# Performance work log

Measured on AMD Instinct MI355X. Metric: run time of the kernel, lower is better.

## Reference

```python
import jax, jax.numpy as jnp
import numpy as np

B, L, HID, NH, HD = 1, 2304, 3072, 24, 128
IMG = 2048
MLP = 4 * HID  # 12288
EPS = 1e-6


def _layernorm(x):
    mu = jnp.mean(x, axis=-1, keepdims=True)
    var = jnp.mean(jnp.square(x - mu), axis=-1, keepdims=True)
    return (x - mu) * jax.lax.rsqrt(var + EPS)


def _rmsnorm(x, w):
    ms = jnp.mean(jnp.square(x), axis=-1, keepdims=True)
    return x * jax.lax.rsqrt(ms + EPS) * w


def _rope_interleaved(x, cos, sin):
    # x: [B, S, H, D]; cos/sin: [1, S, 1, D] with pairwise-equal values (mode=1, GPT-J)
    x1 = x[..., 0::2]
    x2 = x[..., 1::2]
    c = cos[..., 0::2]
    s = sin[..., 0::2]
    even = x1 * c - x2 * s
    odd = x1 * s + x2 * c
    return jnp.stack([even, odd], axis=-1).reshape(x.shape)


def setup_inputs() -> dict:
    key = jax.random.key(0)
    ks = jax.random.split(key, 10)
    scale_in = 1.0 / np.sqrt(HID)
    x = jax.random.normal(ks[0], (B, L, HID), jnp.float32)
    vec = jax.random.normal(ks[1], (B, HID), jnp.float32)
    # RoPE tables (interleaved layout: value repeated per pair)
    pos = jnp.arange(IMG, dtype=jnp.float32)
    inv_freq = 1.0 / (10000.0 ** (jnp.arange(HD // 2, dtype=jnp.float32) / (HD // 2)))
    ang = pos[:, None] * inv_freq[None, :]               # [IMG, HD/2]
    freqs_cos = jnp.repeat(jnp.cos(ang), 2, axis=-1).reshape(1, IMG, 1, HD)
    freqs_sin = jnp.repeat(jnp.sin(ang), 2, axis=-1).reshape(1, IMG, 1, HD)
    mod_w = jax.random.normal(ks[2], (HID, 3 * HID), jnp.float32) * scale_in
    mod_b = jnp.zeros((3 * HID,), jnp.float32)
    w1 = jax.random.normal(ks[3], (HID, 3 * HID + MLP), jnp.float32) * scale_in
    b1 = jnp.zeros((3 * HID + MLP,), jnp.float32)
    q_norm_w = jnp.ones((HD,), jnp.float32)
    k_norm_w = jnp.ones((HD,), jnp.float32)
    w2 = jax.random.normal(ks[4], (HID + MLP, HID), jnp.float32) * (1.0 / np.sqrt(HID + MLP))
    b2 = jnp.zeros((HID,), jnp.float32)
    return {
        'x': x, 'vec': vec, 'img_len': IMG,
        'freqs_cos': freqs_cos, 'freqs_sin': freqs_sin,
        'mod_w': mod_w, 'mod_b': mod_b, 'w1': w1, 'b1': b1,
        'q_norm_w': q_norm_w, 'k_norm_w': k_norm_w, 'w2': w2, 'b2': b2,
    }


def reference(x, vec, img_len, freqs_cos, freqs_sin, mod_w, mod_b, w1, b1,
              q_norm_w, k_norm_w, w2, b2):
    # modulation: SiLU(vec) -> Linear -> shift/scale/gate  [B, HID] each
    mod = jax.nn.silu(vec) @ mod_w + mod_b
    shift, scale, gate = jnp.split(mod, 3, axis=-1)
    x_mod = _layernorm(x) * (1.0 + scale[:, None, :]) + shift[:, None, :]

    # fused QKV + MLP projection
    proj = x_mod @ w1 + b1                                  # [B, L, 3*HID + MLP]
    qkv, mlp = proj[..., :3 * HID], proj[..., 3 * HID:]
    q, k, v = [t[:, :, 0] for t in [None]] if False else None, None, None
    qkv = qkv.reshape(B, L, 3, NH, HD)
    q, k, v = qkv[:, :, 0], qkv[:, :, 1], qkv[:, :, 2]      # [B, L, NH, HD]

    q = _rmsnorm(q, q_norm_w)
    k = _rmsnorm(k, k_norm_w)

    # RoPE only on image tokens
    q = jnp.concatenate([_rope_interleaved(q[:, :img_len], freqs_cos, freqs_sin), q[:, img_len:]], axis=1)
    k = jnp.concatenate([_rope_interleaved(k[:, :img_len], freqs_cos, freqs_sin), k[:, img_len:]], axis=1)

    # full (img+txt) bidirectional attention
    attn_scale = 1.0 / np.sqrt(HD)
    scores = jnp.einsum('blhd,bmhd->bhlm', q, k) * attn_scale
    probs = jax.nn.softmax(scores, axis=-1)
    attn = jnp.einsum('bhlm,bmhd->blhd', probs, v).reshape(B, L, NH * HD)

    # output fusion: [attn | gelu_tanh(mlp)] @ w2
    out = jnp.concatenate([attn, jax.nn.gelu(mlp, approximate=True)], axis=-1) @ w2 + b2
    return x + out * gate[:, None, :]
```

## Files before the change

kernel.cpp:

```cpp
#include <hip/hip_runtime.h>

#define L_SEQ 2304
#define HID_D 3072
#define NH_D 24
#define HD_D 128
#define N1_D 21504
#define QKVN 9216
#define K2_D 15360
#define EPS_V 1e-6f
#define ATTN_SC 0.08838834764831843f

typedef __bf16 bf16x8 __attribute__((ext_vector_type(8)));
typedef float f32x4 __attribute__((ext_vector_type(4)));
typedef unsigned int u32x4 __attribute__((ext_vector_type(4)));
typedef unsigned short u16x8 __attribute__((ext_vector_type(8)));
typedef unsigned short u16x4 __attribute__((ext_vector_type(4)));

#define WAITVM(N) asm volatile("s_waitcnt vmcnt(" #N ")" ::: "memory")
#define LGKM0 asm volatile("s_waitcnt lgkmcnt(0)" ::: "memory")
#define SB0 __builtin_amdgcn_sched_barrier(0)

__device__ __forceinline__ unsigned short f2bf(float f) {
  unsigned int u = __builtin_bit_cast(unsigned int, f);
  u += 0x7fffu + ((u >> 16) & 1u);
  return (unsigned short)(u >> 16);
}

__device__ __forceinline__ float gelu_f(float x) {
  float u = 0.7978845608028654f * (x + 0.044715f * x * x * x);
  float e = __expf(2.f * u);
  float th = 1.f - 2.f / (e + 1.f);
  return 0.5f * x * (1.f + th);
}

__device__ __forceinline__ void gload16(const void* g, void* l) {
  __builtin_amdgcn_global_load_lds(
      (const __attribute__((address_space(1))) unsigned int*)g,
      (__attribute__((address_space(3))) unsigned int*)l, 16, 0, 0);
}

__global__ __launch_bounds__(256) void mod_partial_kernel(
    const float* __restrict__ vec, const float* __restrict__ mod_w,
    float* __restrict__ partial) {
  __shared__ float s[384];
  const int t = threadIdx.x;
  const int kb = blockIdx.y;
  const int k0 = kb * 384;
  for (int p = t; p < 384; p += 256) {
    float v = vec[k0 + p];
    s[p] = v / (1.f + __expf(-v));
  }
  __syncthreads();
  const int n = blockIdx.x * 256 + t;
  float acc = 0.f;
  const float* wp = mod_w + (size_t)k0 * QKVN + n;
#pragma unroll 4
  for (int j = 0; j < 384; ++j) acc += s[j] * wp[(size_t)j * QKVN];
  partial[kb * QKVN + n] = acc;
}

__global__ __launch_bounds__(256) void mod_reduce_kernel(
    const float* __restrict__ partial, const float* __restrict__ mod_b,
    float* __restrict__ mod) {
  const int n = blockIdx.x * 256 + threadIdx.x;
  float acc = mod_b[n];
#pragma unroll
  for (int i = 0; i < 8; ++i) acc += partial[i * QKVN + n];
  mod[n] = acc;
}

__global__ __launch_bounds__(256) void ln_mod_kernel(
    const float* __restrict__ x, const float* __restrict__ mod,
    unsigned short* __restrict__ xmod) {
  const int row = blockIdx.x;
  const int t = threadIdx.x;
  const float* xr = x + (size_t)row * HID_D;
  float4 v[3];
  float sum = 0.f, sq = 0.f;
#pragma unroll
  for (int p = 0; p < 3; ++p) {
    v[p] = *(const float4*)&xr[p * 1024 + t * 4];
    sum += v[p].x + v[p].y + v[p].z + v[p].w;
    sq += v[p].x * v[p].x + v[p].y * v[p].y + v[p].z * v[p].z + v[p].w * v[p].w;
  }
#pragma unroll
  for (int o = 1; o < 64; o <<= 1) {
    sum += __shfl_xor(sum, o);
    sq += __shfl_xor(sq, o);
  }
  __shared__ float rs[8];
  const int w = t >> 6;
  if ((t & 63) == 0) { rs[w] = sum; rs[4 + w] = sq; }
  __syncthreads();
  sum = rs[0] + rs[1] + rs[2] + rs[3];
  sq = rs[4] + rs[5] + rs[6] + rs[7];
  const float mu = sum * (1.f / HID_D);
  const float var = sq * (1.f / HID_D) - mu * mu;
  const float rstd = rsqrtf(var + EPS_V);
#pragma unroll
  for (int p = 0; p < 3; ++p) {
    const int c = p * 1024 + t * 4;
    float4 sc = *(const float4*)&mod[3072 + c];
    float4 sh = *(const float4*)&mod[c];
    u16x4 o4;
    o4[0] = f2bf((v[p].x - mu) * rstd * (1.f + sc.x) + sh.x);
    o4[1] = f2bf((v[p].y - mu) * rstd * (1.f + sc.y) + sh.y);
    o4[2] = f2bf((v[p].z - mu) * rstd * (1.f + sc.z) + sh.z);
    o4[3] = f2bf((v[p].w - mu) * rstd * (1.f + sc.w) + sh.w);
    *(u16x4*)&xmod[(size_t)row * HID_D + c] = o4;
  }
}

__global__ __launch_bounds__(256) void convert_transpose_kernel(
    const float* __restrict__ src, unsigned short* __restrict__ dst,
    const int K, const int N) {
  __shared__ unsigned short lt[64][72];
  const int t = threadIdx.x;
  const int n0 = blockIdx.x * 64;
  const int k0 = blockIdx.y * 64;
  const int kr = t >> 4;
  const int n4 = (t & 15) * 4;
#pragma unroll
  for (int p = 0; p < 4; ++p) {
    const int k = kr + p * 16;
    float4 v = *(const float4*)&src[(size_t)(k0 + k) * N + n0 + n4];
    lt[n4 + 0][k] = f2bf(v.x);
    lt[n4 + 1][k] = f2bf(v.y);
    lt[n4 + 2][k] = f2bf(v.z);
    lt[n4 + 3][k] = f2bf(v.w);
  }
  __syncthreads();
  const int nr = t >> 2;
  const int kc = (t & 3) * 16;
  u16x8 a = *(const u16x8*)&lt[nr][kc];
  u16x8 b = *(const u16x8*)&lt[nr][kc + 8];
  unsigned short* dp = &dst[(size_t)(n0 + nr) * K + k0 + kc];
  *(u16x8*)dp = a;
  *(u16x8*)(dp + 8) = b;
}

template <int BM>
__device__ __forceinline__ void gemm8_core(
    const unsigned short* __restrict__ A, const int lda,
    const unsigned short* __restrict__ B, const int ldb,
    const int m0, const int n0, const int nit, char* lds,
    f32x4 (*acc)[4]) {
  constexpr int AB = BM * 128;
  constexpr int AH = AB / 2;
  constexpr int BO = 2 * AB;
  constexpr int ALOADS = BM / 128;

  const int t = threadIdx.x;
  const int lane = t & 63;
  const int w = t >> 6;
  const int g = lane >> 4;
  const int c = lane & 15;
  const int wm = (w >> 2) * (BM / 2);
  const int wn = (w & 3) * 64;
  const int srow = w * 16 + (lane >> 2);
  const int scole = (lane & 3) * 8;

  auto stageA = [&](int buf, int kh, int kt) {
#pragma unroll
    for (int j = 0; j < ALOADS; ++j)
      gload16(A + (size_t)(m0 + j * 128 + srow) * lda + kt * 64 + kh * 32 + scole,
              lds + buf * AB + kh * AH + j * 8192 + w * 1024);
  };
  auto stageB = [&](int buf, int kh, int kt) {
#pragma unroll
    for (int j = 0; j < 2; ++j)
      gload16(B + (size_t)(n0 + j * 128 + srow) * ldb + kt * 64 + kh * 32 + scole,
              lds + BO + buf * 32768 + kh * 16384 + j * 8192 + w * 1024);
  };

  bf16x8 af[4], bf[4];
  auto loadA = [&](int buf, int mh, int kk) {
    const char* base = lds + buf * AB + kk * AH;
#pragma unroll
    for (int i = 0; i < 4; ++i)
      af[i] = *(const bf16x8*)(base + (wm + (mh * 4 + i) * 16 + c) * 64 + g * 16);
  };
  auto loadB4 = [&](int buf, int kk) {
    const char* base = lds + BO + buf * 32768 + kk * 16384;
#pragma unroll
    for (int i = 0; i < 4; ++i)
      bf[i] = *(const bf16x8*)(base + (wn + i * 16 + c) * 64 + g * 16);
  };
  auto loadB2 = [&](int buf, int hi, int kk) {
    const char* base = lds + BO + buf * 32768 + kk * 16384;
#pragma unroll
    for (int i = 0; i < 2; ++i)
      bf[hi * 2 + i] =
          *(const bf16x8*)(base + (wn + (hi * 2 + i) * 16 + c) * 64 + g * 16);
  };
  auto mfma16 = [&](int mb) {
#pragma unroll
    for (int i = 0; i < 4; ++i)
#pragma unroll
      for (int n = 0; n < 4; ++n)
        acc[mb + i][n] = __builtin_amdgcn_mfma_f32_16x16x32_bf16(
            af[i], bf[n], acc[mb + i][n], 0, 0, 0);
  };
  auto mfma8 = [&](int hi) {
#pragma unroll
    for (int i = 0; i < 4; ++i)
#pragma unroll
      for (int n = 0; n < 2; ++n)
        acc[i][hi * 2 + n] = __builtin_amdgcn_mfma_f32_16x16x32_bf16(
            af[i], bf[hi * 2 + n], acc[i][hi * 2 + n], 0, 0, 0);
  };
  auto mid = [&] {
    SB0;
    __builtin_amdgcn_s_barrier();
    LGKM0;
    SB0;
    __builtin_amdgcn_s_setprio(1);
  };
  auto end_nw = [&] {
    __builtin_amdgcn_s_setprio(0);
    SB0;
    __builtin_amdgcn_s_barrier();
  };

  stageA(0, 0, 0); stageB(0, 0, 0);
  stageA(0, 1, 0); stageB(0, 1, 0);
  stageA(1, 0, 1); stageB(1, 0, 1);
  if constexpr (BM == 256) WAITVM(8); else WAITVM(6);
  __builtin_amdgcn_s_barrier();

  for (int it = 0; it < nit; ++it) {
    const int t0 = 2 * it;
    const bool nl = (it + 1 < nit);
    if constexpr (BM == 256) { loadA(0, 0, 0); loadB4(0, 0); }
    else { loadA(0, 0, 0); loadB2(0, 0, 0); }
    stageA(1, 1, t0 + 1);
    mid();
    if constexpr (BM == 256) mfma16(0); else mfma8(0);
    end_nw();
    if constexpr (BM == 256) loadA(0, 1, 0); else loadB2(0, 1, 0);
    stageB(1, 1, t0 + 1);
    mid();
    if constexpr (BM == 256) mfma16(4); else mfma8(1);
    __builtin_amdgcn_s_setprio(0); SB0;
    if constexpr (BM == 256) WAITVM(8); else WAITVM(6);
    __builtin_amdgcn_s_barrier();
    if constexpr (BM == 256) { loadA(0, 0, 1); loadB4(0, 1); }
    else { loadA(0, 0, 1); loadB2(0, 0, 1); }
    if (nl) stageA(0, 0, t0 + 2);
    mid();
    if constexpr (BM == 256) mfma16(0); else mfma8(0);
    end_nw();
    if constexpr (BM == 256) loadA(0, 1, 1); else loadB2(0, 1, 1);
    if (nl) stageB(0, 0, t0 + 2);
    mid();
    if constexpr (BM == 256) mfma16(4); else mfma8(1);
    __builtin_amdgcn_s_setprio(0); SB0;
    if (nl) { if constexpr (BM == 256) WAITVM(8); else WAITVM(6); }
    else    { if constexpr (BM == 256) WAITVM(4); else WAITVM(3); }
    __builtin_amdgcn_s_barrier();
    if constexpr (BM == 256) { loadA(1, 0, 0); loadB4(1, 0); }
    else { loadA(1, 0, 0); loadB2(1, 0, 0); }
    if (nl) stageA(0, 1, t0 + 2);
    mid();
    if constexpr (BM == 256) mfma16(0); else mfma8(0);
    end_nw();
    if constexpr (BM == 256) loadA(1, 1, 0); else loadB2(1, 1, 0);
    if (nl) stageB(0, 1, t0 + 2);
    mid();
    if constexpr (BM == 256) mfma16(4); else mfma8(1);
    __builtin_amdgcn_s_setprio(0); SB0;
    if (nl) { if constexpr (BM == 256) WAITVM(8); else WAITVM(6); }
    else    { WAITVM(0); }
    __builtin_amdgcn_s_barrier();
    if constexpr (BM == 256) { loadA(1, 0, 1); loadB4(1, 1); }
    else { loadA(1, 0, 1); loadB2(1, 0, 1); }
    if (nl) stageA(1, 0, t0 + 3);
    mid();
    if constexpr (BM == 256) mfma16(0); else mfma8(0);
    end_nw();
    if constexpr (BM == 256) loadA(1, 1, 1); else loadB2(1, 1, 1);
    if (nl) stageB(1, 0, t0 + 3);
    mid();
    if constexpr (BM == 256) mfma16(4); else mfma8(1);
    __builtin_amdgcn_s_setprio(0); SB0;
    if (nl) { if constexpr (BM == 256) WAITVM(8); else WAITVM(6); }
    __builtin_amdgcn_s_barrier();
  }
}

__global__ __launch_bounds__(512, 2) void gemm1_kernel(
    const unsigned short* __restrict__ xmod, const unsigned short* __restrict__ w1t,
    const float* __restrict__ b1, float* __restrict__ qkv,
    unsigned short* __restrict__ hbuf) {
  __shared__ __align__(16) char smem[131072];
  f32x4 acc[8][4];
  const f32x4 zero = {0.f, 0.f, 0.f, 0.f};
#pragma unroll
  for (int i = 0; i < 8; ++i)
#pragma unroll
    for (int j = 0; j < 4; ++j) acc[i][j] = zero;
  const int orig = blockIdx.x;
  const int xcd = orig & 7;
  const int wgid = (xcd < 4 ? xcd * 95 : 380 + (xcd - 4) * 94) + (orig >> 3);
  const int m0 = (wgid % 9) * 256;
  const int n0 = (wgid / 9) * 256;
  gemm8_core<256>(xmod, HID_D, w1t, HID_D, m0, n0, 24, smem, acc);
  const int lane = threadIdx.x & 63;
  const int g = lane >> 4, c = lane & 15;
  const int w = threadIdx.x >> 6;
  const int wm = (w >> 2) * 128, wn = (w & 3) * 64;
  const bool is_mlp = (n0 >= QKVN);
#pragma unroll
  for (int mf = 0; mf < 8; ++mf)
#pragma unroll
    for (int nf = 0; nf < 4; ++nf)
#pragma unroll
      for (int j = 0; j < 4; ++j) {
        const int row = m0 + wm + mf * 16 + g * 4 + j;
        const int col = n0 + wn + nf * 16 + c;
        const float v = acc[mf][nf][j] + b1[col];
        if (!is_mlp) {
          qkv[(size_t)row * QKVN + col] = v;
        } else {
          hbuf[(size_t)row * K2_D + HID_D + (col - QKVN)] = f2bf(gelu_f(v));
        }
      }
}

__global__ __launch_bounds__(512, 2) void gemm2_kernel(
    const unsigned short* __restrict__ hbuf, const unsigned short* __restrict__ w2t,
    const float* __restrict__ b2, const float* __restrict__ x,
    const float* __restrict__ mod, float* __restrict__ out) {
  __shared__ __align__(16) char smem[98304];
  f32x4 acc[4][4];
  const f32x4 zero = {0.f, 0.f, 0.f, 0.f};
#pragma unroll
  for (int i = 0; i < 4; ++i)
#pragma unroll
    for (int j = 0; j < 4; ++j) acc[i][j] = zero;
  const int orig = blockIdx.x;
  const int wgid = (orig & 7) * 27 + (orig >> 3);
  const int m0 = (wgid % 18) * 128;
  const int n0 = (wgid / 18) * 256;
  gemm8_core<128>(hbuf, K2_D, w2t, K2_D, m0, n0, 120, smem, acc);
  const int lane = threadIdx.x & 63;
  const int g = lane >> 4, c = lane & 15;
  const int w = threadIdx.x >> 6;
  const int wm = (w >> 2) * 64, wn = (w & 3) * 64;
#pragma unroll
  for (int mf = 0; mf < 4; ++mf)
#pragma unroll
    for (int nf = 0; nf < 4; ++nf)
#pragma unroll
      for (int j = 0; j < 4; ++j) {
        const int row = m0 + wm + mf * 16 + g * 4 + j;
        const int col = n0 + wn + nf * 16 + c;
        const float v = acc[mf][nf][j] + b2[col];
        out[(size_t)row * HID_D + col] =
            x[(size_t)row * HID_D + col] + v * mod[6144 + col];
      }
}

__global__ __launch_bounds__(256) void qk_norm_rope_kernel(
    const float* __restrict__ qkv, const float* __restrict__ qw,
    const float* __restrict__ kw, const float* __restrict__ fc,
    const float* __restrict__ fs, const int* __restrict__ img_len_p,
    unsigned short* __restrict__ qr, unsigned short* __restrict__ kr) {
  const int l = blockIdx.x;
  const int t = threadIdx.x;
  const int wv = t >> 6;
  const int lane = t & 63;
  const int img = *img_len_p;
  const bool do_rope = (l < img);
  float cc = 1.f, ss = 0.f;
  if (do_rope) {
    cc = fc[l * HD_D + 2 * lane];
    ss = fs[l * HD_D + 2 * lane];
  }
  const float qw0 = qw[2 * lane], qw1 = qw[2 * lane + 1];
  const float kw0 = kw[2 * lane], kw1 = kw[2 * lane + 1];
#pragma unroll
  for (int hh = 0; hh < 6; ++hh) {
    const int h = hh * 4 + wv;
    {
      float2 q2 = *(const float2*)&qkv[(size_t)l * QKVN + h * HD_D + 2 * lane];
      float sq = q2.x * q2.x + q2.y * q2.y;
#pragma unroll
      for (int o = 1; o < 64; o <<= 1) sq += __shfl_xor(sq, o);
      const float r = rsqrtf(sq * (1.f / HD_D) + EPS_V);
      float a = q2.x * r * qw0, b = q2.y * r * qw1;
      float e = a, od = b;
      if (do_rope) { e = a * cc - b * ss; od = a * ss + b * cc; }
      e *= ATTN_SC; od *= ATTN_SC;
      unsigned int pk = (unsigned)f2bf(e) | ((unsigned)f2bf(od) << 16);
      *(unsigned int*)&qr[((size_t)h * L_SEQ + l) * HD_D + 2 * lane] = pk;
    }
    {
      float2 k2 = *(const float2*)&qkv[(size_t)l * QKVN + HID_D + h * HD_D + 2 * lane];
      float sq = k2.x * k2.x + k2.y * k2.y;
#pragma unroll
      for (int o = 1; o < 64; o <<= 1) sq += __shfl_xor(sq, o);
      const float r = rsqrtf(sq * (1.f / HD_D) + EPS_V);
      float a = k2.x * r * kw0, b = k2.y * r * kw1;
      float e = a, od = b;
      if (do_rope) { e = a * cc - b * ss; od = a * ss + b * cc; }
      unsigned int pk = (unsigned)f2bf(e) | ((unsigned)f2bf(od) << 16);
      *(unsigned int*)&kr[((size_t)h * L_SEQ + l) * HD_D + 2 * lane] = pk;
    }
  }
}

__global__ __launch_bounds__(256) void v_transpose_kernel(
    const float* __restrict__ qkv, unsigned short* __restrict__ vT) {
  __shared__ unsigned short lv[128 * 64];
  const int h = blockIdx.y;
  const int l0 = blockIdx.x * 64;
  const int t = threadIdx.x;
#pragma unroll
  for (int p = 0; p < 8; ++p) {
    const int idx = p * 256 + t;
    const int l = idx >> 5;
    const int d4 = (idx & 31) * 4;
    float4 v = *(const float4*)&qkv[(size_t)(l0 + l) * QKVN + 2 * HID_D + h * HD_D + d4];
    const unsigned sw = (unsigned)(((d4 >> 2) & 7) << 4);
    *(unsigned short*)((char*)lv + (((d4 + 0) * 128 + 2 * l) ^ sw)) = f2bf(v.x);
    *(unsigned short*)((char*)lv + (((d4 + 1) * 128 + 2 * l) ^ sw)) = f2bf(v.y);
    *(unsigned short*)((char*)lv + (((d4 + 2) * 128 + 2 * l) ^ sw)) = f2bf(v.z);
    *(unsigned short*)((char*)lv + (((d4 + 3) * 128 + 2 * l) ^ sw)) = f2bf(v.w);
  }
  __syncthreads();
  const int d = t >> 1;
  const int half = t & 1;
  const unsigned swr = (unsigned)(((d >> 2) & 7) << 4);
#pragma unroll
  for (int j2 = 0; j2 < 4; ++j2) {
    u32x4 v = *(const u32x4*)((const char*)lv + ((d * 128 + half * 64 + j2 * 16) ^ swr));
    *(u32x4*)&vT[(size_t)(h * HD_D + d) * L_SEQ + l0 + half * 32 + j2 * 8] = v;
  }
}

__global__ __launch_bounds__(256) void attn_kernel(
    const unsigned short* __restrict__ qr, const unsigned short* __restrict__ kr,
    const unsigned short* __restrict__ vT, unsigned short* __restrict__ hbuf) {
  __shared__ unsigned short lds_k[64 * 128];
  __shared__ unsigned short lds_v[128 * 64];
  __shared__ unsigned short lds_p[4 * 16 * 64];
  const int hidx = blockIdx.y;
  const int l0 = blockIdx.x * 64;
  const int t = threadIdx.x;
  const int lane = t & 63;
  const int w = t >> 6;
  const int g = lane >> 4;
  const int c = lane & 15;

  bf16x8 qa[4];
  {
    const unsigned short* qrow = qr + ((size_t)hidx * L_SEQ + l0 + w * 16 + c) * HD_D;
#pragma unroll
    for (int ks = 0; ks < 4; ++ks)
      qa[ks] = *(const bf16x8*)&qrow[ks * 32 + g * 8];
  }
  f32x4 acc[8];
  const f32x4 zero = {0.f, 0.f, 0.f, 0.f};
#pragma unroll
  for (int i = 0; i < 8; ++i) acc[i] = zero;
  float m_r[4] = {-1e30f, -1e30f, -1e30f, -1e30f};
  float l_r[4] = {0.f, 0.f, 0.f, 0.f};

  for (int kv0 = 0; kv0 < L_SEQ; kv0 += 64) {
    __syncthreads();
#pragma unroll
    for (int p = 0; p < 4; ++p) {
      const int idx = p * 256 + t;
      const int r = idx >> 4, ch = idx & 15;
      u32x4 v = *(const u32x4*)&kr[((size_t)hidx * L_SEQ + kv0 + r) * HD_D + ch * 8];
      *(u32x4*)((char*)lds_k + ((r * 256 + ch * 16) ^ ((r & 7) << 4))) = v;
    }
#pragma unroll
    for (int p = 0; p < 4; ++p) {
      const int idx = p * 256 + t;
      const int d_ = idx >> 3, ch = idx & 7;
      u32x4 v = *(const u32x4*)&vT[(size_t)(hidx * HD_D + d_) * L_SEQ + kv0 + ch * 8];
      *(u32x4*)((char*)lds_v + ((d_ * 128 + ch * 16) ^ ((d_ & 7) << 4))) = v;
    }
    __syncthreads();
    f32x4 s[4];
#pragma unroll
    for (int cf = 0; cf < 4; ++cf) s[cf] = zero;
#pragma unroll
    for (int ks = 0; ks < 4; ++ks) {
      const int kb = (ks * 32 + g * 8) * 2;
#pragma unroll
      for (int cf = 0; cf < 4; ++cf) {
        const int kvr = cf * 16 + c;
        bf16x8 kf = *(const bf16x8*)((const char*)lds_k + ((kvr * 256 + kb) ^ ((kvr & 7) << 4)));
        s[cf] = __builtin_amdgcn_mfma_f32_16x16x32_bf16(qa[ks], kf, s[cf], 0, 0, 0);
      }
    }
    float pv[4][4];
    float alpha[4];
#pragma unroll
    for (int r = 0; r < 4; ++r) {
      float mx = fmaxf(fmaxf(s[0][r], s[1][r]), fmaxf(s[2][r], s[3][r]));
      mx = fmaxf(mx, __shfl_xor(mx, 1));
      mx = fmaxf(mx, __shfl_xor(mx, 2));
      mx = fmaxf(mx, __shfl_xor(mx, 4));
      mx = fmaxf(mx, __shfl_xor(mx, 8));
      const float mnew = fmaxf(m_r[r], mx);
      alpha[r] = __expf(m_r[r] - mnew);
      float rsum = 0.f;
#pragma unroll
      for (int cf = 0; cf < 4; ++cf) {
        const float p_ = __expf(s[cf][r] - mnew);
        pv[cf][r] = p_;
        rsum += p_;
      }
      rsum += __shfl_xor(rsum, 1);
      rsum += __shfl_xor(rsum, 2);
      rsum += __shfl_xor(rsum, 4);
      rsum += __shfl_xor(rsum, 8);
      l_r[r] = l_r[r] * alpha[r] + rsum;
      m_r[r] = mnew;
    }
#pragma unroll
    for (int of = 0; of < 8; ++of)
#pragma unroll
      for (int r = 0; r < 4; ++r) acc[of][r] *= alpha[r];
#pragma unroll
    for (int cf = 0; cf < 4; ++cf)
#pragma unroll
      for (int r = 0; r < 4; ++r) {
        const int row = g * 4 + r;
        const int col = cf * 16 + c;
        *(unsigned short*)((char*)lds_p +
                           ((w * 2048 + row * 128 + col * 2) ^ ((row & 7) << 4))) =
            f2bf(pv[cf][r]);
      }
    asm volatile("s_waitcnt lgkmcnt(0)" ::: "memory");
    __builtin_amdgcn_sched_barrier(0);
#pragma unroll
    for (int ks = 0; ks < 2; ++ks) {
      bf16x8 pa = *(const bf16x8*)((const char*)lds_p +
                                   ((w * 2048 + c * 128 + (ks * 32 + g * 8) * 2) ^
                                    ((c & 7) << 4)));
#pragma unroll
      for (int of = 0; of < 8; ++of) {
        const int dcol = of * 16 + c;
        bf16x8 vb = *(const bf16x8*)((const char*)lds_v +
                                     ((dcol * 128 + (ks * 32 + g * 8) * 2) ^
                                      ((dcol & 7) << 4)));
        acc[of] = __builtin_amdgcn_mfma_f32_16x16x32_bf16(pa, vb, acc[of], 0, 0, 0);
      }
    }
  }
#pragma unroll
  for (int of = 0; of < 8; ++of)
#pragma unroll
    for (int r = 0; r < 4; ++r) {
      const int row = l0 + w * 16 + g * 4 + r;
      const int col = hidx * HD_D + of * 16 + c;
      hbuf[(size_t)row * K2_D + col] = f2bf(acc[of][r] / l_r[r]);
    }
}

extern "C" void kernel_launch(void* const* d_in, const int* in_sizes, int n_in,
                              void* d_out, int out_size, void* d_ws, size_t ws_size,
                              hipStream_t stream) {
  (void)in_sizes; (void)n_in; (void)out_size; (void)ws_size;
  const float* x = (const float*)d_in[0];
  const float* vec = (const float*)d_in[1];
  const int* img_len = (const int*)d_in[2];
  const float* fc = (const float*)d_in[3];
  const float* fs = (const float*)d_in[4];
  const float* mod_w = (const float*)d_in[5];
  const float* mod_b = (const float*)d_in[6];
  const float* w1 = (const float*)d_in[7];
  const float* b1 = (const float*)d_in[8];
  const float* qw = (const float*)d_in[9];
  const float* kw = (const float*)d_in[10];
  const float* w2 = (const float*)d_in[11];
  const float* b2 = (const float*)d_in[12];
  float* out = (float*)d_out;

  char* wsb = (char*)d_ws;
  float* mod = (float*)(wsb + 0);
  float* partial = (float*)(wsb + 36864);
  unsigned short* xmod = (unsigned short*)(wsb + 331776);
  float* qkv = (float*)(wsb + 14487552);
  unsigned short* hbuf = (unsigned short*)(wsb + 99422208);
  unsigned short* qr = (unsigned short*)(wsb + 170201088);
  unsigned short* kr = (unsigned short*)(wsb + 184356864);
  unsigned short* vT = (unsigned short*)(wsb + 198512640);
  unsigned short* wt = (unsigned short*)(wsb + 212668416);

  mod_partial_kernel<<<dim3(36, 8), 256, 0, stream>>>(vec, mod_w, partial);
  mod_reduce_kernel<<<36, 256, 0, stream>>>(partial, mod_b, mod);
  ln_mod_kernel<<<2304, 256, 0, stream>>>(x, mod, xmod);
  convert_transpose_kernel<<<dim3(N1_D / 64, HID_D / 64), 256, 0, stream>>>(
      w1, wt, HID_D, N1_D);
  gemm1_kernel<<<756, 512, 0, stream>>>(xmod, wt, b1, qkv, hbuf);
  convert_transpose_kernel<<<dim3(HID_D / 64, K2_D / 64), 256, 0, stream>>>(
      w2, wt, K2_D, HID_D);
  qk_norm_rope_kernel<<<2304, 256, 0, stream>>>(qkv, qw, kw, fc, fs, img_len, qr, kr);
  v_transpose_kernel<<<dim3(36, 24), 256, 0, stream>>>(qkv, vT);
  attn_kernel<<<dim3(36, 24), 256, 0, stream>>>(qr, kr, vT, hbuf);
  gemm2_kernel<<<216, 512, 0, stream>>>(hbuf, wt, b2, x, mod, out);
}
```

Measured before the change: 1.027 ms.

## Restructure GEMM core with XOR-swizzled full-K64 LDS tiles and quadrant MFMA schedule

Rewrites the shared GEMM core so each staged LDS row holds a full 64-wide K slice (128 bytes) with an XOR swizzle on 16-byte chunks, replacing the two 32-wide K halves. Each wave now computes its output as four quadrants, reusing B fragments across quadrant pairs (bq0/bq1), and stages are split by row group instead of K half. The intent is to cut LDS bank conflicts and the number of barriers and ds_read issues per K step. The vmcnt waits and staging order change accordingly, which risks stalls or a mistimed pipeline if the counts are wrong.

```diff
diff --git a/kernel.cpp b/kernel.cpp
--- a/kernel.cpp
+++ b/kernel.cpp
@@ -143,147 +143,125 @@
 __device__ __forceinline__ void gemm8_core(
     const unsigned short* __restrict__ A, const int lda,
     const unsigned short* __restrict__ B, const int ldb,
-    const int m0, const int n0, const int nit, char* lds,
-    f32x4 (*acc)[4]) {
-  constexpr int AB = BM * 128;
-  constexpr int AH = AB / 2;
-  constexpr int BO = 2 * AB;
-  constexpr int ALOADS = BM / 128;
+    const int m0, const int n0, const int nit, char* lds, f32x4 (*acc)[4]) {
+  constexpr int AREG = (BM == 256) ? 16384 : 8192;
+  constexpr int ABUF = 2 * AREG;
+  constexpr int BOFF = 2 * ABUF;
+  constexpr int BREG = 16384;
+  constexpr int BBUF = 32768;
+  constexpr int AROWS = (BM == 256) ? 128 : 64;
+  constexpr int AI = (BM == 256) ? 2 : 1;
+  constexpr int MF = (BM == 256) ? 4 : 2;
+  constexpr int QM = (BM == 256) ? 64 : 32;
 
   const int t = threadIdx.x;
   const int lane = t & 63;
   const int w = t >> 6;
   const int g = lane >> 4;
   const int c = lane & 15;
-  const int wm = (w >> 2) * (BM / 2);
-  const int wn = (w & 3) * 64;
-  const int srow = w * 16 + (lane >> 2);
-  const int scole = (lane & 3) * 8;
-
-  auto stageA = [&](int buf, int kh, int kt) {
-#pragma unroll
-    for (int j = 0; j < ALOADS; ++j)
-      gload16(A + (size_t)(m0 + j * 128 + srow) * lda + kt * 64 + kh * 32 + scole,
-              lds + buf * AB + kh * AH + j * 8192 + w * 1024);
-  };
-  auto stageB = [&](int buf, int kh, int kt) {
-#pragma unroll
-    for (int j = 0; j < 2; ++j)
-      gload16(B + (size_t)(n0 + j * 128 + srow) * ldb + kt * 64 + kh * 32 + scole,
-              lds + BO + buf * 32768 + kh * 16384 + j * 8192 + w * 1024);
-  };
-
-  bf16x8 af[4], bf[4];
-  auto loadA = [&](int buf, int mh, int kk) {
-    const char* base = lds + buf * AB + kk * AH;
-#pragma unroll
-    for (int i = 0; i < 4; ++i)
-      af[i] = *(const bf16x8*)(base + (wm + (mh * 4 + i) * 16 + c) * 64 + g * 16);
-  };
-  auto loadB4 = [&](int buf, int kk) {
-    const char* base = lds + BO + buf * 32768 + kk * 16384;
-#pragma unroll
-    for (int i = 0; i < 4; ++i)
-      bf[i] = *(const bf16x8*)(base + (wn + i * 16 + c) * 64 + g * 16);
-  };
-  auto loadB2 = [&](int buf, int hi, int kk) {
-    const char* base = lds + BO + buf * 32768 + kk * 16384;
+  const int sr8 = lane >> 3;
+  const int scol = ((lane & 7) ^ sr8) * 8;
+  const int arg = w >> 2;
+  const int brg = (w & 3) >> 1;
+  const int bbase = (w & 1) * 64;
+
+  auto stageA = [&](int buf, int rg, int kt) {
+#pragma unroll
+    for (int i = 0; i < AI; ++i)
+      gload16(A + (size_t)(m0 + rg * AROWS + i * 64 + w * 8 + sr8) * lda +
+                  kt * 64 + scol,
+              lds + buf * ABUF + rg * AREG + i * 8192 + w * 1024);
+  };
+  auto stageB = [&](int buf, int rg, int kt) {
 #pragma unroll
     for (int i = 0; i < 2; ++i)
-      bf[hi * 2 + i] =
-          *(const bf16x8*)(base + (wn + (hi * 2 + i) * 16 + c) * 64 + g * 16);
-  };
-  auto mfma16 = [&](int mb) {
-#pragma unroll
-    for (int i = 0; i < 4; ++i)
-#pragma unroll
-      for (int n = 0; n < 4; ++n)
-        acc[mb + i][n] = __builtin_amdgcn_mfma_f32_16x16x32_bf16(
-            af[i], bf[n], acc[mb + i][n], 0, 0, 0);
-  };
-  auto mfma8 = [&](int hi) {
-#pragma unroll
-    for (int i = 0; i < 4; ++i)
+      gload16(B + (size_t)(n0 + rg * 128 + i * 64 + w * 8 + sr8) * ldb +
+                  kt * 64 + scol,
+              lds + BOFF + buf * BBUF + rg * BREG + i * 8192 + w * 1024);
+  };
+
+  bf16x8 af[2 * MF], bq0[4], bq1[4];
+  auto ldA = [&](int buf, int qm) {
+    const char* ab = lds + buf * ABUF + arg * AREG;
+#pragma unroll
+    for (int i = 0; i < MF; ++i) {
+      const int lr = qm * QM + i * 16 + c;
+#pragma unroll
+      for (int kk = 0; kk < 2; ++kk)
+        af[i * 2 + kk] =
+            *(const bf16x8*)(ab + lr * 128 + (((kk * 4 + g) ^ (c & 7)) << 4));
+    }
+  };
+  auto ldB = [&](int buf, int qn, bf16x8* bq) {
+    const char* bb = lds + BOFF + buf * BBUF + brg * BREG;
+#pragma unroll
+    for (int i = 0; i < 2; ++i) {
+      const int lr = bbase + qn * 32 + i * 16 + c;
+#pragma unroll
+      for (int kk = 0; kk < 2; ++kk)
+        bq[i * 2 + kk] =
+            *(const bf16x8*)(bb + lr * 128 + (((kk * 4 + g) ^ (c & 7)) << 4));
+    }
+  };
+  auto domf = [&](int qm, int qn, const bf16x8* bq) {
+#pragma unroll
+    for (int i = 0; i < MF; ++i)
 #pragma unroll
       for (int n = 0; n < 2; ++n)
-        acc[i][hi * 2 + n] = __builtin_amdgcn_mfma_f32_16x16x32_bf16(
-            af[i], bf[hi * 2 + n], acc[i][hi * 2 + n], 0, 0, 0);
-  };
-  auto mid = [&] {
+#pragma unroll
+        for (int kk = 0; kk < 2; ++kk)
+          acc[qm * MF + i][qn * 2 + n] = __builtin_amdgcn_mfma_f32_16x16x32_bf16(
+              af[i * 2 + kk], bq[n * 2 + kk], acc[qm * MF + i][qn * 2 + n], 0, 0, 0);
+  };
+  auto MID = [&] {
     SB0;
     __builtin_amdgcn_s_barrier();
     LGKM0;
     SB0;
     __builtin_amdgcn_s_setprio(1);
   };
-  auto end_nw = [&] {
+  auto END = [&] {
     __builtin_amdgcn_s_setprio(0);
     SB0;
     __builtin_amdgcn_s_barrier();
   };
 
-  stageA(0, 0, 0); stageB(0, 0, 0);
-  stageA(0, 1, 0); stageB(0, 1, 0);
-  stageA(1, 0, 1); stageB(1, 0, 1);
-  if constexpr (BM == 256) WAITVM(8); else WAITVM(6);
+  stageB(0, 0, 0); stageA(0, 0, 0); stageB(0, 1, 0); stageA(0, 1, 0);
+  stageB(1, 0, 1); stageA(1, 0, 1);
+  if constexpr (BM == 256) WAITVM(4); else WAITVM(3);
   __builtin_amdgcn_s_barrier();
 
-  for (int it = 0; it < nit; ++it) {
-    const int t0 = 2 * it;
-    const bool nl = (it + 1 < nit);
-    if constexpr (BM == 256) { loadA(0, 0, 0); loadB4(0, 0); }
-    else { loadA(0, 0, 0); loadB2(0, 0, 0); }
-    stageA(1, 1, t0 + 1);
-    mid();
-    if constexpr (BM == 256) mfma16(0); else mfma8(0);
-    end_nw();
-    if constexpr (BM == 256) loadA(0, 1, 0); else loadB2(0, 1, 0);
-    stageB(1, 1, t0 + 1);
-    mid();
-    if constexpr (BM == 256) mfma16(4); else mfma8(1);
+  for (int j = 0; j < nit; ++j) {
+    const int ta = 2 * j;
+    const bool nl = (j + 1 < nit);
+    ldA(0, 0); ldB(0, 0, bq0);
+    stageB(1, 1, ta + 1);
+    MID(); domf(0, 0, bq0); END();
+    ldB(0, 1, bq1);
+    stageA(1, 1, ta + 1);
+    MID(); domf(0, 1, bq1); END();
+    ldA(0, 1);
+    if (nl) stageB(0, 0, ta + 2);
+    MID(); domf(1, 1, bq1); END();
+    if (nl) stageA(0, 0, ta + 2);
+    MID(); domf(1, 0, bq0);
     __builtin_amdgcn_s_setprio(0); SB0;
-    if constexpr (BM == 256) WAITVM(8); else WAITVM(6);
+    if (nl) { if constexpr (BM == 256) WAITVM(4); else WAITVM(3); }
+    else WAITVM(0);
     __builtin_amdgcn_s_barrier();
-    if constexpr (BM == 256) { loadA(0, 0, 1); loadB4(0, 1); }
-    else { loadA(0, 0, 1); loadB2(0, 0, 1); }
-    if (nl) stageA(0, 0, t0 + 2);
-    mid();
-    if constexpr (BM == 256) mfma16(0); else mfma8(0);
-    end_nw();
-    if constexpr (BM == 256) loadA(0, 1, 1); else loadB2(0, 1, 1);
-    if (nl) stageB(0, 0, t0 + 2);
-    mid();
-    if constexpr (BM == 256) mfma16(4); else mfma8(1);
+    ldA(1, 0); ldB(1, 0, bq0);
+    if (nl) stageB(0, 1, ta + 2);
+    MID(); domf(0, 0, bq0); END();
+    ldB(1, 1, bq1);
+    if (nl) stageA(0, 1, ta + 2);
+    MID(); domf(0, 1, bq1); END();
+    ldA(1, 1);
+    if (nl) stageB(1, 0, ta + 3);
+    MID(); domf(1, 1, bq1); END();
+    if (nl) stageA(1, 0, ta + 3);
+    MID(); domf(1, 0, bq0);
     __builtin_amdgcn_s_setprio(0); SB0;
-    if (nl) { if constexpr (BM == 256) WAITVM(8); else WAITVM(6); }
-    else    { if constexpr (BM == 256) WAITVM(4); else WAITVM(3); }
-    __builtin_amdgcn_s_barrier();
-    if constexpr (BM == 256) { loadA(1, 0, 0); loadB4(1, 0); }
-    else { loadA(1, 0, 0); loadB2(1, 0, 0); }
-    if (nl) stageA(0, 1, t0 + 2);
-    mid();
-    if constexpr (BM == 256) mfma16(0); else mfma8(0);
-    end_nw();
-    if constexpr (BM == 256) loadA(1, 1, 0); else loadB2(1, 1, 0);
-    if (nl) stageB(0, 1, t0 + 2);
-    mid();
-    if constexpr (BM == 256) mfma16(4); else mfma8(1);
-    __builtin_amdgcn_s_setprio(0); SB0;
-    if (nl) { if constexpr (BM == 256) WAITVM(8); else WAITVM(6); }
-    else    { WAITVM(0); }
-    __builtin_amdgcn_s_barrier();
-    if constexpr (BM == 256) { loadA(1, 0, 1); loadB4(1, 1); }
-    else { loadA(1, 0, 1); loadB2(1, 0, 1); }
-    if (nl) stageA(1, 0, t0 + 3);
-    mid();
-    if constexpr (BM == 256) mfma16(0); else mfma8(0);
-    end_nw();
-    if constexpr (BM == 256) loadA(1, 1, 1); else loadB2(1, 1, 1);
-    if (nl) stageB(1, 0, t0 + 3);
-    mid();
-    if constexpr (BM == 256) mfma16(4); else mfma8(1);
-    __builtin_amdgcn_s_setprio(0); SB0;
-    if (nl) { if constexpr (BM == 256) WAITVM(8); else WAITVM(6); }
+    if (nl) { if constexpr (BM == 256) WAITVM(4); else WAITVM(3); }
     __builtin_amdgcn_s_barrier();
   }
 }
```

Result: faster. 935.7 us (-8.9%).
